# Optimization experiments

Measured on AMD Instinct MI355X. Metric: run time of the kernel, lower is better.

The kernel has to match this reference:

```python
import jax, jax.numpy as jnp
import numpy as np

N = 50000      # nodes (full graph: num_dst == num_src == N)
E = 800000     # edges, avg degree 16
D = 128        # in_feats == n_hidden == out_feats
L = 3          # n_layers
EPS = 1e-5     # BatchNorm1d eps


def setup_inputs() -> dict:
    key = jax.random.key(0)
    ks = jax.random.split(key, 6)
    feat = jax.random.normal(ks[0], (N, D), dtype=jnp.float32)
    src = jax.random.randint(ks[1], (E,), 0, N)
    dst = jax.random.randint(ks[2], (E,), 0, N)
    scale = 1.0 / np.sqrt(D)
    W_self = jax.random.normal(ks[3], (L, D, D), dtype=jnp.float32) * scale
    W_neigh = jax.random.normal(ks[4], (L, D, D), dtype=jnp.float32) * scale
    b = jax.random.normal(ks[5], (L, D), dtype=jnp.float32) * 0.01
    gamma = jnp.ones((L - 1, D), dtype=jnp.float32)
    beta = jnp.zeros((L - 1, D), dtype=jnp.float32)
    return {"feat": feat, "src": src, "dst": dst, "W_self": W_self,
            "W_neigh": W_neigh, "b": b, "gamma": gamma, "beta": beta}


def reference(feat, src, dst, W_self, W_neigh, b, gamma, beta):
    n = feat.shape[0]
    n_layers = W_self.shape[0]
    # in-degree of each dst node, clamped to 1 (zero-degree nodes aggregate 0)
    deg = jax.ops.segment_sum(jnp.ones_like(dst, dtype=feat.dtype), dst,
                              num_segments=n)
    deg = jnp.maximum(deg, 1.0)[:, None]                      # [N,1]
    h = feat
    for i in range(n_layers):
        # mean aggregation over incoming neighbors: gather + segment-sum
        agg = jax.ops.segment_sum(h[src], dst, num_segments=n) / deg  # [N,D]
        # SAGEConv('mean'): fc_self(h_dst) + fc_neigh(agg) + bias
        hn = h @ W_self[i] + agg @ W_neigh[i] + b[i]
        hn = hn + h                                           # residual (dims match)
        if i < n_layers - 1:
            mu = jnp.mean(hn, axis=0)
            var = jnp.var(hn, axis=0)                         # biased, as BN training
            hn = (hn - mu) * jax.lax.rsqrt(var + EPS) * gamma[i] + beta[i]
            hn = jax.nn.relu(hn)
        h = hn
    return h
```

## Files before the change

kernel.cpp:

```cpp
#include <hip/hip_runtime.h>

#define DIM 128
#define EPSF 1e-5f
#define BK_SHIFT 10
#define BK_NODES 1024
#define BK_CAP 20480

typedef __attribute__((ext_vector_type(8))) short short8;
typedef __attribute__((ext_vector_type(4))) float float4v;

__device__ inline unsigned short f2bf(float x) {
    union { float f; unsigned u; } z; z.f = x;
    unsigned u = z.u;
    unsigned r = u + 0x7FFF + ((u >> 16) & 1);
    return (unsigned short)(r >> 16);
}
__device__ inline float bf2f(unsigned short u) {
    union { unsigned u; float f; } z; z.u = ((unsigned)u) << 16;
    return z.f;
}

__global__ void binA_kernel(const int* __restrict__ src, const int* __restrict__ dst,
                            unsigned* __restrict__ barr, int* __restrict__ bcnt,
                            int E, int NB) {
    __shared__ int cnt[64];
    __shared__ int gcur[64];
    int tid = threadIdx.x;
    int tile0 = blockIdx.x * 4096;
    if (tid < 64) cnt[tid] = 0;
    __syncthreads();
    unsigned pk[16]; int bk[16];
#pragma unroll
    for (int i = 0; i < 16; ++i) {
        int e = tile0 + i * 256 + tid;
        if (e < E) {
            int d = dst[e];
            int s = src[e];
            bk[i] = d >> BK_SHIFT;
            pk[i] = ((unsigned)(d & (BK_NODES - 1)) << 16) | (unsigned)s;
            atomicAdd(&cnt[bk[i]], 1);
        } else bk[i] = -1;
    }
    __syncthreads();
    if (tid < 64) {
        int c = (tid < NB) ? cnt[tid] : 0;
        gcur[tid] = (c > 0) ? atomicAdd(&bcnt[tid], c) : 0;
    }
    __syncthreads();
#pragma unroll
    for (int i = 0; i < 16; ++i) {
        if (bk[i] >= 0) {
            int pos = atomicAdd(&gcur[bk[i]], 1);
            if (pos < BK_CAP)
                barr[(size_t)bk[i] * BK_CAP + pos] = pk[i];
        }
    }
}

__global__ void binB_kernel(const unsigned* __restrict__ barr, const int* __restrict__ bcnt,
                            int* __restrict__ rowptr, int* __restrict__ colidx,
                            int N, int E, int NB) {
    __shared__ int hist[BK_NODES];
    __shared__ int sm[256];
    __shared__ int bc[64];
    __shared__ int gbS;
    int b = blockIdx.x;
    int tid = threadIdx.x;
    if (tid < 64) bc[tid] = (tid < NB) ? bcnt[tid] : 0;
    __syncthreads();
    if (tid == 0) {
        int run = 0;
        for (int i = 0; i < b; ++i) run += bc[i];
        gbS = run;
        if (b == 0) rowptr[N] = E;
    }
    __syncthreads();
    int cnt = bc[b];
    if (cnt > BK_CAP) cnt = BK_CAP;
    const unsigned* arr = barr + (size_t)b * BK_CAP;
    int gb = gbS;
#pragma unroll
    for (int j = 0; j < 4; ++j) hist[tid * 4 + j] = 0;
    __syncthreads();
    for (int i = tid; i < cnt; i += 256)
        atomicAdd(&hist[arr[i] >> 16], 1);
    __syncthreads();
    int h[4], s = 0;
#pragma unroll
    for (int j = 0; j < 4; ++j) { h[j] = hist[tid * 4 + j]; s += h[j]; }
    sm[tid] = s;
    __syncthreads();
    int tot = s;
    for (int off = 1; off < 256; off <<= 1) {
        int x = (tid >= off) ? sm[tid - off] : 0;
        __syncthreads();
        sm[tid] += x;
        __syncthreads();
    }
    int run = sm[tid] - tot;
#pragma unroll
    for (int j = 0; j < 4; ++j) { hist[tid * 4 + j] = run; run += h[j]; }
    __syncthreads();
    int nbase = b << BK_SHIFT;
    int nn = N - nbase; if (nn > BK_NODES) nn = BK_NODES;
    for (int j = tid; j < nn; j += 256)
        rowptr[nbase + j] = gb + hist[j];
    __syncthreads();
    for (int i = tid; i < cnt; i += 256) {
        unsigned u = arr[i];
        int pos = atomicAdd(&hist[u >> 16], 1);
        colidx[gb + pos] = (int)(u & 0xFFFFu);
    }
}

__global__ void packw_kernel(const float* __restrict__ Ws, const float* __restrict__ Wn,
                             unsigned short* __restrict__ wpack) {
    int l = blockIdx.x >> 3;
    int s = blockIdx.x & 7;
    int tid = threadIdx.x;
#pragma unroll
    for (int pi = 0; pi < 2; ++pi) {
        int p = tid * 2 + pi;
        int nt = p >> 6;
        int lane = p & 63;
        int kb = s * 32 + (lane >> 4) * 8;
        int col = nt * 16 + (lane & 15);
        unsigned short* dstp = wpack + (size_t)l * 32768 + ((size_t)(s * 8 + nt) * 64 + lane) * 8;
#pragma unroll
        for (int j = 0; j < 8; ++j) {
            int k = kb + j;
            float v = (k < 128) ? Ws[(size_t)l * 16384 + k * 128 + col]
                                : Wn[(size_t)l * 16384 + (k - 128) * 128 + col];
            dstp[j] = f2bf(v);
        }
    }
}

__global__ void convert_kernel(const float* __restrict__ feat, unsigned short* __restrict__ Acat,
                               int N) {
    int idx = blockIdx.x * blockDim.x + threadIdx.x;
    if (idx >= N * 32) return;
    float4 v = ((const float4*)feat)[idx];
    int r = idx >> 5, c4 = idx & 31;
    ushort4 o;
    o.x = f2bf(v.x); o.y = f2bf(v.y); o.z = f2bf(v.z); o.w = f2bf(v.w);
    ((ushort4*)Acat)[(size_t)r * 64 + c4] = o;
}

__global__ void aggregate_kernel(unsigned short* Acat, const int* __restrict__ rowptr,
                                 const int* __restrict__ colidx, float* __restrict__ stats,
                                 int N) {
    if (blockIdx.x == 0) stats[threadIdx.x] = 0.f;
    int wid = (blockIdx.x * blockDim.x + threadIdx.x) >> 6;
    if (wid >= N) return;
    int lane = threadIdx.x & 63;
    int half = lane >> 5, sl = lane & 31;
    int beg = rowptr[wid], end = rowptr[wid + 1];
    float4 acc = make_float4(0.f, 0.f, 0.f, 0.f);
    int e = beg + half;
    for (; e + 6 < end; e += 8) {
        int s0 = colidx[e];
        int s1 = colidx[e + 2];
        int s2 = colidx[e + 4];
        int s3 = colidx[e + 6];
        ushort4 u0 = *(const ushort4*)(Acat + (size_t)s0 * 256 + sl * 4);
        ushort4 u1 = *(const ushort4*)(Acat + (size_t)s1 * 256 + sl * 4);
        ushort4 u2 = *(const ushort4*)(Acat + (size_t)s2 * 256 + sl * 4);
        ushort4 u3 = *(const ushort4*)(Acat + (size_t)s3 * 256 + sl * 4);
        acc.x += (bf2f(u0.x) + bf2f(u1.x)) + (bf2f(u2.x) + bf2f(u3.x));
        acc.y += (bf2f(u0.y) + bf2f(u1.y)) + (bf2f(u2.y) + bf2f(u3.y));
        acc.z += (bf2f(u0.z) + bf2f(u1.z)) + (bf2f(u2.z) + bf2f(u3.z));
        acc.w += (bf2f(u0.w) + bf2f(u1.w)) + (bf2f(u2.w) + bf2f(u3.w));
    }
    for (; e < end; e += 2) {
        int s0 = colidx[e];
        ushort4 u0 = *(const ushort4*)(Acat + (size_t)s0 * 256 + sl * 4);
        acc.x += bf2f(u0.x);
        acc.y += bf2f(u0.y);
        acc.z += bf2f(u0.z);
        acc.w += bf2f(u0.w);
    }
    acc.x += __shfl_xor(acc.x, 32);
    acc.y += __shfl_xor(acc.y, 32);
    acc.z += __shfl_xor(acc.z, 32);
    acc.w += __shfl_xor(acc.w, 32);
    if (half == 0) {
        int deg = end - beg;
        float inv = 1.0f / (float)(deg > 0 ? deg : 1);
        ushort4 o;
        o.x = f2bf(acc.x * inv); o.y = f2bf(acc.y * inv);
        o.z = f2bf(acc.z * inv); o.w = f2bf(acc.w * inv);
        *(ushort4*)(Acat + (size_t)wid * 256 + 128 + sl * 4) = o;
    }
}

__launch_bounds__(256)
__global__ void gemm_kernel(const unsigned short* __restrict__ Acat,
                            const unsigned short* __restrict__ wpack,
                            const float* __restrict__ bias,
                            unsigned short* __restrict__ outb, float* __restrict__ outf,
                            float* __restrict__ stats, int withStats, int N) {
    __shared__ unsigned short Bs[32768];
    int tid = threadIdx.x;
    {
        const float4* wsrc = (const float4*)wpack;
        float4* bdst = (float4*)Bs;
#pragma unroll
        for (int i = 0; i < 16; ++i) bdst[i * 256 + tid] = wsrc[i * 256 + tid];
    }
    __syncthreads();

    int wave = tid >> 6, lane = tid & 63;
    int row0 = blockIdx.x * 128 + wave * 32;
    int mrow = lane & 15, kq = lane >> 4;
    const unsigned short* Abase = Acat + (size_t)(row0 + mrow) * 256 + kq * 8;

    float4v acc[2][8];
#pragma unroll
    for (int i = 0; i < 2; ++i)
#pragma unroll
        for (int j = 0; j < 8; ++j) acc[i][j] = (float4v){0.f, 0.f, 0.f, 0.f};

#pragma unroll
    for (int s = 0; s < 8; ++s) {
        short8 a0 = *(const short8*)(Abase + s * 32);
        short8 a1 = *(const short8*)(Abase + 16 * 256 + s * 32);
#pragma unroll
        for (int nt = 0; nt < 8; ++nt) {
            short8 b = *(const short8*)(Bs + ((size_t)(s * 8 + nt) * 64 + lane) * 8);
            acc[0][nt] = __builtin_amdgcn_mfma_f32_16x16x32_bf16(a0, b, acc[0][nt], 0, 0, 0);
            acc[1][nt] = __builtin_amdgcn_mfma_f32_16x16x32_bf16(a1, b, acc[1][nt], 0, 0, 0);
        }
    }

    float* sm = (float*)Bs;
    if (withStats) {
        __syncthreads();
        sm[tid] = 0.f;
        __syncthreads();
    }

    int colb = lane & 15;
    int rq = (lane >> 4) * 4;
#pragma unroll
    for (int mt = 0; mt < 2; ++mt) {
        int rowt = row0 + mt * 16 + rq;
#pragma unroll
        for (int nt = 0; nt < 8; ++nt) {
            int col = nt * 16 + colb;
            float bv = bias[col];
            float slo = 0.f, qlo = 0.f;
#pragma unroll
            for (int r = 0; r < 4; ++r) {
                int row = rowt + r;
                if (row < N) {
                    float res = bf2f(Acat[(size_t)row * 256 + col]);
                    float v = acc[mt][nt][r] + bv + res;
                    if (withStats) {
                        outb[(size_t)row * 128 + col] = f2bf(v);
                        slo += v; qlo += v * v;
                    } else {
                        outf[(size_t)row * 128 + col] = v;
                    }
                }
            }
            if (withStats) {
                atomicAdd(&sm[col], slo);
                atomicAdd(&sm[128 + col], qlo);
            }
        }
    }
    if (withStats) {
        __syncthreads();
        if (tid < 128) {
            atomicAdd(&stats[tid], sm[tid]);
            atomicAdd(&stats[128 + tid], sm[128 + tid]);
        }
    }
}

__global__ void bnapply_kernel(const unsigned short* __restrict__ hn,
                               unsigned short* __restrict__ Acat,
                               const float* __restrict__ stats, const float* __restrict__ gamma,
                               const float* __restrict__ beta, float invN, int N) {
    __shared__ float sc_s[128], sh_s[128];
    int tid = threadIdx.x;
    if (tid < 128) {
        float mean = stats[tid] * invN;
        float var = stats[128 + tid] * invN - mean * mean;
        float sc = gamma[tid] * rsqrtf(var + EPSF);
        sc_s[tid] = sc;
        sh_s[tid] = beta[tid] - mean * sc;
    }
    __syncthreads();
    int idx = blockIdx.x * 256 + tid;
    if (idx >= N * 32) return;
    int row = idx >> 5, c4 = idx & 31;
    ushort4 u = *(const ushort4*)(hn + (size_t)idx * 4);
    ushort4 o;
    {
        int col = c4 * 4;
        float v0 = fmaf(bf2f(u.x), sc_s[col], sh_s[col]);
        float v1 = fmaf(bf2f(u.y), sc_s[col + 1], sh_s[col + 1]);
        float v2 = fmaf(bf2f(u.z), sc_s[col + 2], sh_s[col + 2]);
        float v3 = fmaf(bf2f(u.w), sc_s[col + 3], sh_s[col + 3]);
        o.x = f2bf(fmaxf(v0, 0.f));
        o.y = f2bf(fmaxf(v1, 0.f));
        o.z = f2bf(fmaxf(v2, 0.f));
        o.w = f2bf(fmaxf(v3, 0.f));
    }
    *(ushort4*)(Acat + (size_t)row * 256 + c4 * 4) = o;
}

extern "C" void kernel_launch(void* const* d_in, const int* in_sizes, int n_in,
                              void* d_out, int out_size, void* d_ws, size_t ws_size,
                              hipStream_t stream) {
    const float* feat  = (const float*)d_in[0];
    const int*   src   = (const int*)d_in[1];
    const int*   dst   = (const int*)d_in[2];
    const float* Wself = (const float*)d_in[3];
    const float* Wneig = (const float*)d_in[4];
    const float* bias  = (const float*)d_in[5];
    const float* gamma = (const float*)d_in[6];
    const float* beta  = (const float*)d_in[7];

    int N = in_sizes[0] / DIM;
    int E = in_sizes[1];
    int Npad = (N + 127) & ~127;
    int NB = (N + BK_NODES - 1) >> BK_SHIFT;

    char* ws = (char*)d_ws;
    size_t off = 0;
    auto alloc = [&](size_t bytes) -> void* {
        void* p = ws + off;
        off = (off + bytes + 255) & ~(size_t)255;
        return p;
    };
    unsigned short* Acat   = (unsigned short*)alloc((size_t)Npad * 256 * 2);
    unsigned short* hnS    = (unsigned short*)alloc((size_t)Npad * 128 * 2);
    unsigned short* wpack  = (unsigned short*)alloc((size_t)3 * 32768 * 2);
    int*   colidx = (int*)alloc((size_t)E * 4);
    int*   rowptr = (int*)alloc((size_t)(N + 1) * 4);
    int*   bcnt   = (int*)alloc(64 * 4);
    float* stats  = (float*)alloc(256 * 4);

    unsigned* barr = (unsigned*)Acat;

    hipMemsetAsync(bcnt, 0, 64 * 4, stream);
    binA_kernel<<<(E + 4095) / 4096, 256, 0, stream>>>(src, dst, barr, bcnt, E, NB);
    binB_kernel<<<NB, 256, 0, stream>>>(barr, bcnt, rowptr, colidx, N, E, NB);

    packw_kernel<<<24, 256, 0, stream>>>(Wself, Wneig, wpack);
    convert_kernel<<<(N * 32 + 255) / 256, 256, 0, stream>>>(feat, Acat, N);
    if (Npad > N)
        hipMemsetAsync(Acat + (size_t)N * 256, 0, (size_t)(Npad - N) * 512, stream);

    float invN = 1.0f / (float)N;

    for (int l = 0; l < 3; ++l) {
        aggregate_kernel<<<(N + 3) / 4, 256, 0, stream>>>(Acat, rowptr, colidx, stats, N);
        int withStats = (l < 2) ? 1 : 0;
        gemm_kernel<<<Npad / 128, 256, 0, stream>>>(
            Acat, wpack + (size_t)l * 32768, bias + (size_t)l * DIM,
            hnS, (float*)d_out, stats, withStats, N);
        if (withStats)
            bnapply_kernel<<<(N * 32 + 255) / 256, 256, 0, stream>>>(
                hnS, Acat, stats, gamma + (size_t)l * DIM, beta + (size_t)l * DIM, invN, N);
    }
}
```

Before: 356.3 us.

## Fuse neighbor aggregation into GEMM kernel with swizzled LDS aggregate tile

```diff
diff --git a/kernel.cpp b/kernel.cpp
--- a/kernel.cpp
+++ b/kernel.cpp
@@ -7,6 +7,7 @@
 #define BK_CAP 20480
 
 typedef __attribute__((ext_vector_type(8))) short short8;
+typedef __attribute__((ext_vector_type(8))) unsigned short ushort8;
 typedef __attribute__((ext_vector_type(4))) float float4v;
 
 __device__ inline unsigned short f2bf(float x) {
@@ -136,84 +137,74 @@
     }
 }
 
-__global__ void convert_kernel(const float* __restrict__ feat, unsigned short* __restrict__ Acat,
+__global__ void convert_kernel(const float* __restrict__ feat, unsigned short* __restrict__ Hb,
                                int N) {
     int idx = blockIdx.x * blockDim.x + threadIdx.x;
     if (idx >= N * 32) return;
     float4 v = ((const float4*)feat)[idx];
-    int r = idx >> 5, c4 = idx & 31;
     ushort4 o;
     o.x = f2bf(v.x); o.y = f2bf(v.y); o.z = f2bf(v.z); o.w = f2bf(v.w);
-    ((ushort4*)Acat)[(size_t)r * 64 + c4] = o;
-}
-
-__global__ void aggregate_kernel(unsigned short* Acat, const int* __restrict__ rowptr,
-                                 const int* __restrict__ colidx, float* __restrict__ stats,
-                                 int N) {
-    if (blockIdx.x == 0) stats[threadIdx.x] = 0.f;
-    int wid = (blockIdx.x * blockDim.x + threadIdx.x) >> 6;
-    if (wid >= N) return;
-    int lane = threadIdx.x & 63;
-    int half = lane >> 5, sl = lane & 31;
-    int beg = rowptr[wid], end = rowptr[wid + 1];
-    float4 acc = make_float4(0.f, 0.f, 0.f, 0.f);
-    int e = beg + half;
-    for (; e + 6 < end; e += 8) {
-        int s0 = colidx[e];
-        int s1 = colidx[e + 2];
-        int s2 = colidx[e + 4];
-        int s3 = colidx[e + 6];
-        ushort4 u0 = *(const ushort4*)(Acat + (size_t)s0 * 256 + sl * 4);
-        ushort4 u1 = *(const ushort4*)(Acat + (size_t)s1 * 256 + sl * 4);
-        ushort4 u2 = *(const ushort4*)(Acat + (size_t)s2 * 256 + sl * 4);
-        ushort4 u3 = *(const ushort4*)(Acat + (size_t)s3 * 256 + sl * 4);
-        acc.x += (bf2f(u0.x) + bf2f(u1.x)) + (bf2f(u2.x) + bf2f(u3.x));
-        acc.y += (bf2f(u0.y) + bf2f(u1.y)) + (bf2f(u2.y) + bf2f(u3.y));
-        acc.z += (bf2f(u0.z) + bf2f(u1.z)) + (bf2f(u2.z) + bf2f(u3.z));
-        acc.w += (bf2f(u0.w) + bf2f(u1.w)) + (bf2f(u2.w) + bf2f(u3.w));
-    }
-    for (; e < end; e += 2) {
-        int s0 = colidx[e];
-        ushort4 u0 = *(const ushort4*)(Acat + (size_t)s0 * 256 + sl * 4);
-        acc.x += bf2f(u0.x);
-        acc.y += bf2f(u0.y);
-        acc.z += bf2f(u0.z);
-        acc.w += bf2f(u0.w);
-    }
-    acc.x += __shfl_xor(acc.x, 32);
-    acc.y += __shfl_xor(acc.y, 32);
-    acc.z += __shfl_xor(acc.z, 32);
-    acc.w += __shfl_xor(acc.w, 32);
-    if (half == 0) {
-        int deg = end - beg;
+    ((ushort4*)Hb)[idx] = o;
+}
+
+__launch_bounds__(256)
+__global__ void fusedgemm_kernel(const unsigned short* __restrict__ Hb,
+                                 const int* __restrict__ rowptr,
+                                 const int* __restrict__ colidx,
+                                 const unsigned short* __restrict__ wpack,
+                                 const float* __restrict__ bias,
+                                 unsigned short* __restrict__ outb, float* __restrict__ outf,
+                                 float* __restrict__ stats, int withStats, int N) {
+    __shared__ __align__(16) unsigned short aggT[128 * 128];
+    __shared__ float sm[256];
+    int tid = threadIdx.x;
+    int wave = tid >> 6, lane = tid & 63;
+    int row0 = blockIdx.x * 128;
+    sm[tid] = 0.f;
+    __syncthreads();
+
+    int q = lane >> 4;
+    int ql = lane & 15;
+    for (int i = 0; i < 8; ++i) {
+        int lrow = (wave << 5) + (q << 3) + i;
+        int node = row0 + lrow;
+        float a[8];
+#pragma unroll
+        for (int j = 0; j < 8; ++j) a[j] = 0.f;
+        int deg = 1;
+        if (node < N) {
+            int beg = rowptr[node], end = rowptr[node + 1];
+            deg = end - beg;
+            int e = beg;
+            for (; e + 3 < end; e += 4) {
+                int s0 = colidx[e], s1 = colidx[e + 1], s2 = colidx[e + 2], s3 = colidx[e + 3];
+                ushort8 u0 = *(const ushort8*)(Hb + (size_t)s0 * 128 + ql * 8);
+                ushort8 u1 = *(const ushort8*)(Hb + (size_t)s1 * 128 + ql * 8);
+                ushort8 u2 = *(const ushort8*)(Hb + (size_t)s2 * 128 + ql * 8);
+                ushort8 u3 = *(const ushort8*)(Hb + (size_t)s3 * 128 + ql * 8);
+#pragma unroll
+                for (int j = 0; j < 8; ++j)
+                    a[j] += (bf2f((unsigned short)u0[j]) + bf2f((unsigned short)u1[j]))
+                          + (bf2f((unsigned short)u2[j]) + bf2f((unsigned short)u3[j]));
+            }
+            for (; e < end; ++e) {
+                int s0 = colidx[e];
+                ushort8 u0 = *(const ushort8*)(Hb + (size_t)s0 * 128 + ql * 8);
+#pragma unroll
+                for (int j = 0; j < 8; ++j) a[j] += bf2f((unsigned short)u0[j]);
+            }
+        }
         float inv = 1.0f / (float)(deg > 0 ? deg : 1);
-        ushort4 o;
-        o.x = f2bf(acc.x * inv); o.y = f2bf(acc.y * inv);
-        o.z = f2bf(acc.z * inv); o.w = f2bf(acc.w * inv);
-        *(ushort4*)(Acat + (size_t)wid * 256 + 128 + sl * 4) = o;
-    }
-}
-
-__launch_bounds__(256)
-__global__ void gemm_kernel(const unsigned short* __restrict__ Acat,
-                            const unsigned short* __restrict__ wpack,
-                            const float* __restrict__ bias,
-                            unsigned short* __restrict__ outb, float* __restrict__ outf,
-                            float* __restrict__ stats, int withStats, int N) {
-    __shared__ unsigned short Bs[32768];
-    int tid = threadIdx.x;
-    {
-        const float4* wsrc = (const float4*)wpack;
-        float4* bdst = (float4*)Bs;
-#pragma unroll
-        for (int i = 0; i < 16; ++i) bdst[i * 256 + tid] = wsrc[i * 256 + tid];
-    }
-    __syncthreads();
-
-    int wave = tid >> 6, lane = tid & 63;
-    int row0 = blockIdx.x * 128 + wave * 32;
+        ushort8 o;
+#pragma unroll
+        for (int j = 0; j < 8; ++j) o[j] = f2bf(a[j] * inv);
+        unsigned boff = (unsigned)lrow * 256u + (unsigned)ql * 16u;
+        boff ^= (unsigned)((lrow & 7) << 4);
+        *(ushort8*)((char*)aggT + boff) = o;
+    }
+
     int mrow = lane & 15, kq = lane >> 4;
-    const unsigned short* Abase = Acat + (size_t)(row0 + mrow) * 256 + kq * 8;
+    const unsigned short* Sbase = Hb + (size_t)(row0 + (wave << 5) + mrow) * 128 + kq * 8;
 
     float4v acc[2][8];
 #pragma unroll
@@ -223,28 +214,32 @@
 
 #pragma unroll
     for (int s = 0; s < 8; ++s) {
-        short8 a0 = *(const short8*)(Abase + s * 32);
-        short8 a1 = *(const short8*)(Abase + 16 * 256 + s * 32);
+        short8 a0, a1;
+        if (s < 4) {
+            a0 = *(const short8*)(Sbase + s * 32);
+            a1 = *(const short8*)(Sbase + (size_t)16 * 128 + s * 32);
+        } else {
+            int lr0 = (wave << 5) + mrow;
+            int lr1 = lr0 + 16;
+            unsigned c = (unsigned)(((s - 4) * 32 + kq * 8) * 2);
+            unsigned b0 = (unsigned)lr0 * 256u + c; b0 ^= (unsigned)((lr0 & 7) << 4);
+            unsigned b1 = (unsigned)lr1 * 256u + c; b1 ^= (unsigned)((lr1 & 7) << 4);
+            a0 = *(const short8*)((const char*)aggT + b0);
+            a1 = *(const short8*)((const char*)aggT + b1);
+        }
 #pragma unroll
         for (int nt = 0; nt < 8; ++nt) {
-            short8 b = *(const short8*)(Bs + ((size_t)(s * 8 + nt) * 64 + lane) * 8);
+            short8 b = *(const short8*)(wpack + ((size_t)(s * 8 + nt) * 64 + lane) * 8);
             acc[0][nt] = __builtin_amdgcn_mfma_f32_16x16x32_bf16(a0, b, acc[0][nt], 0, 0, 0);
             acc[1][nt] = __builtin_amdgcn_mfma_f32_16x16x32_bf16(a1, b, acc[1][nt], 0, 0, 0);
         }
     }
 
-    float* sm = (float*)Bs;
-    if (withStats) {
-        __syncthreads();
-        sm[tid] = 0.f;
-        __syncthreads();
-    }
-
     int colb = lane & 15;
     int rq = (lane >> 4) * 4;
 #pragma unroll
     for (int mt = 0; mt < 2; ++mt) {
-        int rowt = row0 + mt * 16 + rq;
+        int rowt = row0 + (wave << 5) + mt * 16 + rq;
 #pragma unroll
         for (int nt = 0; nt < 8; ++nt) {
             int col = nt * 16 + colb;
@@ -254,7 +249,7 @@
             for (int r = 0; r < 4; ++r) {
                 int row = rowt + r;
                 if (row < N) {
-                    float res = bf2f(Acat[(size_t)row * 256 + col]);
+                    float res = bf2f(Hb[(size_t)row * 128 + col]);
                     float v = acc[mt][nt][r] + bv + res;
                     if (withStats) {
                         outb[(size_t)row * 128 + col] = f2bf(v);
@@ -280,7 +275,7 @@
 }
 
 __global__ void bnapply_kernel(const unsigned short* __restrict__ hn,
-                               unsigned short* __restrict__ Acat,
+                               unsigned short* __restrict__ Hb,
                                const float* __restrict__ stats, const float* __restrict__ gamma,
                                const float* __restrict__ beta, float invN, int N) {
     __shared__ float sc_s[128], sh_s[128];
@@ -295,7 +290,7 @@
     __syncthreads();
     int idx = blockIdx.x * 256 + tid;
     if (idx >= N * 32) return;
-    int row = idx >> 5, c4 = idx & 31;
+    int c4 = idx & 31;
     ushort4 u = *(const ushort4*)(hn + (size_t)idx * 4);
     ushort4 o;
     {
@@ -309,7 +304,7 @@
         o.z = f2bf(fmaxf(v2, 0.f));
         o.w = f2bf(fmaxf(v3, 0.f));
     }
-    *(ushort4*)(Acat + (size_t)row * 256 + c4 * 4) = o;
+    *(ushort4*)(Hb + (size_t)idx * 4) = o;
 }
 
 extern "C" void kernel_launch(void* const* d_in, const int* in_sizes, int n_in,
@@ -336,35 +331,35 @@
         off = (off + bytes + 255) & ~(size_t)255;
         return p;
     };
-    unsigned short* Acat   = (unsigned short*)alloc((size_t)Npad * 256 * 2);
+    unsigned short* Hb     = (unsigned short*)alloc((size_t)Npad * 128 * 2);
     unsigned short* hnS    = (unsigned short*)alloc((size_t)Npad * 128 * 2);
     unsigned short* wpack  = (unsigned short*)alloc((size_t)3 * 32768 * 2);
     int*   colidx = (int*)alloc((size_t)E * 4);
     int*   rowptr = (int*)alloc((size_t)(N + 1) * 4);
     int*   bcnt   = (int*)alloc(64 * 4);
-    float* stats  = (float*)alloc(256 * 4);
-
-    unsigned* barr = (unsigned*)Acat;
-
-    hipMemsetAsync(bcnt, 0, 64 * 4, stream);
+    float* stats  = (float*)alloc(512 * 4);
+
+    unsigned* barr = (unsigned*)Hb;
+
+    hipMemsetAsync(bcnt, 0, 64 * 4 + 512 * 4, stream);
     binA_kernel<<<(E + 4095) / 4096, 256, 0, stream>>>(src, dst, barr, bcnt, E, NB);
     binB_kernel<<<NB, 256, 0, stream>>>(barr, bcnt, rowptr, colidx, N, E, NB);
 
     packw_kernel<<<24, 256, 0, stream>>>(Wself, Wneig, wpack);
-    convert_kernel<<<(N * 32 + 255) / 256, 256, 0, stream>>>(feat, Acat, N);
+    convert_kernel<<<(N * 32 + 255) / 256, 256, 0, stream>>>(feat, Hb, N);
     if (Npad > N)
-        hipMemsetAsync(Acat + (size_t)N * 256, 0, (size_t)(Npad - N) * 512, stream);
+        hipMemsetAsync(Hb + (size_t)N * 128, 0, (size_t)(Npad - N) * 256, stream);
 
     float invN = 1.0f / (float)N;
 
     for (int l = 0; l < 3; ++l) {
-        aggregate_kernel<<<(N + 3) / 4, 256, 0, stream>>>(Acat, rowptr, colidx, stats, N);
         int withStats = (l < 2) ? 1 : 0;
-        gemm_kernel<<<Npad / 128, 256, 0, stream>>>(
-            Acat, wpack + (size_t)l * 32768, bias + (size_t)l * DIM,
-            hnS, (float*)d_out, stats, withStats, N);
+        fusedgemm_kernel<<<Npad / 128, 256, 0, stream>>>(
+            Hb, rowptr, colidx, wpack + (size_t)l * 32768, bias + (size_t)l * DIM,
+            hnS, (float*)d_out, stats + (size_t)l * 256, withStats, N);
         if (withStats)
             bnapply_kernel<<<(N * 32 + 255) / 256, 256, 0, stream>>>(
-                hnS, Acat, stats, gamma + (size_t)l * DIM, beta + (size_t)l * DIM, invN, N);
-    }
-}
+                hnS, Hb, stats + (size_t)l * 256, gamma + (size_t)l * DIM,
+                beta + (size_t)l * DIM, invN, N);
+    }
+}
```

After: 424.4 us. 1.19x slower.
